# Kernel optimization log

Measured on AMD Instinct MI355X. Metric: run time of the kernel, lower is better.

The kernel has to match this reference:

```python
import jax, jax.numpy as jnp
import numpy as np

N_NODES = 100000
N_EDGES = 1600000
F_IN = 256
HIDDEN = 32
HEADS = 4
N_CLASSES = 16
NEG_SLOPE = 0.2  # PyG GATConv default


def setup_inputs() -> dict:
    key = jax.random.key(0)
    ks = jax.random.split(key, 10)
    x = jax.random.normal(ks[0], (N_NODES, F_IN), dtype=jnp.float32)
    edge_index = jax.random.randint(ks[1], (2, N_EDGES), 0, N_NODES, dtype=jnp.int64)
    # layer 1 params: W1 [F_IN, HEADS*HIDDEN], attention vectors [HEADS, HIDDEN]
    s1 = 1.0 / np.sqrt(F_IN)
    W1 = jax.random.uniform(ks[2], (F_IN, HEADS * HIDDEN), jnp.float32, -s1, s1)
    a_src1 = jax.random.normal(ks[3], (HEADS, HIDDEN), dtype=jnp.float32) * 0.1
    a_dst1 = jax.random.normal(ks[4], (HEADS, HIDDEN), dtype=jnp.float32) * 0.1
    b1 = jnp.zeros((HEADS * HIDDEN,), jnp.float32)
    # layer 2 params: in = HEADS*HIDDEN, out = N_CLASSES, heads=1
    d2 = HEADS * HIDDEN
    s2 = 1.0 / np.sqrt(d2)
    W2 = jax.random.uniform(ks[5], (d2, N_CLASSES), jnp.float32, -s2, s2)
    a_src2 = jax.random.normal(ks[6], (1, N_CLASSES), dtype=jnp.float32) * 0.1
    a_dst2 = jax.random.normal(ks[7], (1, N_CLASSES), dtype=jnp.float32) * 0.1
    b2 = jnp.zeros((N_CLASSES,), jnp.float32)
    return {"x": x, "W1": W1, "a_src1": a_src1, "a_dst1": a_dst1, "b1": b1,
            "W2": W2, "a_src2": a_src2, "a_dst2": a_dst2, "b2": b2,
            "edge_index": edge_index}


def gat_conv(x, src, dst, W, a_src, a_dst, bias, heads, head_dim, concat, num_nodes):
    # linear transform: [N, K, H]
    h = (x @ W).reshape(num_nodes, heads, head_dim)
    # per-node attention logits: [N, K]
    alpha_src = jnp.einsum('nkh,kh->nk', h, a_src)
    alpha_dst = jnp.einsum('nkh,kh->nk', h, a_dst)
    # per-edge scores (message src -> dst): [E, K]
    e = jax.nn.leaky_relu(alpha_src[src] + alpha_dst[dst], NEG_SLOPE)
    # segment softmax grouped by destination node (stable)
    m = jax.ops.segment_max(e, dst, num_segments=num_nodes)
    ex = jnp.exp(e - m[dst])
    denom = jax.ops.segment_sum(ex, dst, num_segments=num_nodes)
    alpha = ex / (denom[dst] + 1e-16)  # [E, K]
    # weighted scatter-add aggregation: [N, K, H]
    msg = h[src] * alpha[:, :, None]
    out = jax.ops.segment_sum(msg, dst, num_segments=num_nodes)
    if concat:
        return out.reshape(num_nodes, heads * head_dim) + bias
    return out.mean(axis=1) + bias


def reference(x, W1, a_src1, a_dst1, b1, W2, a_src2, a_dst2, b2, edge_index):
    n = x.shape[0]
    loops = jnp.arange(n, dtype=edge_index.dtype)
    src = jnp.concatenate([edge_index[0], loops])  # PyG adds self-loops
    dst = jnp.concatenate([edge_index[1], loops])
    # eval mode: feature/attention dropout is identity
    h = gat_conv(x, src, dst, W1, a_src1, a_dst1, b1, HEADS, HIDDEN, True, n)
    h = jax.nn.elu(h)
    out = gat_conv(h, src, dst, W2, a_src2, a_dst2, b2, 1, N_CLASSES, False, n)
    return jax.nn.log_softmax(out, axis=1)
```

## Files before the change

### kernel.cpp

```cpp
#include <hip/hip_runtime.h>
#include <hip/hip_bf16.h>
#include <math.h>

#define N_NODES 100000
#define N_EDGES 1600000
#define EP (N_EDGES + N_NODES)
#define F_IN 256
#define HIDDEN 32
#define HEADS 4
#define D1 (HEADS*HIDDEN)
#define NC 16
#define NEG_SLOPE 0.2f
#define NSTRIP 6250
#define NBUCK 391
#define NCHUNKB 128
#define CHUNK 13312

typedef __attribute__((ext_vector_type(8))) short bf16x8;
typedef __attribute__((ext_vector_type(4))) float f32x4;


__device__ __forceinline__ float lrelu(float x) { return x > 0.f ? x : NEG_SLOPE * x; }

__device__ __forceinline__ unsigned bfpack(float lo, float hi) {
    unsigned a = __float_as_uint(lo), b = __float_as_uint(hi);
    a = (a + 0x7fffu + ((a >> 16) & 1u)) >> 16;
    b = (b + 0x7fffu + ((b >> 16) & 1u)) & 0xffff0000u;
    return a | b;
}
__device__ __forceinline__ unsigned short bf16r(float f) {
    unsigned a = __float_as_uint(f);
    return (unsigned short)((a + 0x7fffu + ((a >> 16) & 1u)) >> 16);
}
__device__ __forceinline__ float bflo(unsigned v) { return __uint_as_float(v << 16); }
__device__ __forceinline__ float bfhi(unsigned v) { return __uint_as_float(v & 0xffff0000u); }

__global__ __launch_bounds__(256) void kA_hist(const int* __restrict__ ei,
                                               unsigned* __restrict__ histG) {
    __shared__ unsigned h[NBUCK];
    const int tid = threadIdx.x;
    for (int i = tid; i < NBUCK; i += 256) h[i] = 0;
    __syncthreads();
    const int base = blockIdx.x * CHUNK;
    const int lim = min(base + CHUNK, EP);
    for (int e = base + tid * 4; e + 3 < lim; e += 1024) {
        if (e < N_EDGES) {
            const int4 d = *(const int4*)(ei + N_EDGES + e);
            atomicAdd(&h[d.x >> 8], 1u);
            atomicAdd(&h[d.y >> 8], 1u);
            atomicAdd(&h[d.z >> 8], 1u);
            atomicAdd(&h[d.w >> 8], 1u);
        } else {
            const int dst = e - N_EDGES;
            atomicAdd(&h[dst >> 8], 1u);
            atomicAdd(&h[(dst + 1) >> 8], 1u);
            atomicAdd(&h[(dst + 2) >> 8], 1u);
            atomicAdd(&h[(dst + 3) >> 8], 1u);
        }
    }
    __syncthreads();
    for (int i = tid; i < NBUCK; i += 256) histG[i * NCHUNKB + blockIdx.x] = h[i];
}

__global__ __launch_bounds__(512) void kB_scan(unsigned* __restrict__ histG,
                                               int* __restrict__ row_ptr) {
    __shared__ unsigned sb[512];
    const int t = threadIdx.x;
    unsigned total = 0;
    if (t < NBUCK) {
        const uint4* p = (const uint4*)(histG + t * NCHUNKB);
        #pragma unroll
        for (int c = 0; c < NCHUNKB / 4; ++c) {
            const uint4 v = p[c];
            total += v.x + v.y + v.z + v.w;
        }
    }
    sb[t] = (t < NBUCK) ? total : 0;
    __syncthreads();
    for (int off = 1; off < 512; off <<= 1) {
        const unsigned u = (t >= off) ? sb[t - off] : 0;
        __syncthreads();
        sb[t] += u;
        __syncthreads();
    }
    if (t < NBUCK) {
        unsigned run = sb[t] - total;
        uint4* p = (uint4*)(histG + t * NCHUNKB);
        #pragma unroll
        for (int c = 0; c < NCHUNKB / 4; ++c) {
            uint4 v = p[c];
            uint4 o;
            o.x = run; run += v.x;
            o.y = run; run += v.y;
            o.z = run; run += v.z;
            o.w = run; run += v.w;
            p[c] = o;
        }
    }
    if (t == 0) row_ptr[N_NODES] = EP;
}

__global__ __launch_bounds__(256) void kC_bucket(const int* __restrict__ ei,
                                                 const unsigned* __restrict__ histG,
                                                 unsigned* __restrict__ packed) {
    __shared__ unsigned cur[NBUCK];
    const int tid = threadIdx.x;
    for (int i = tid; i < NBUCK; i += 256) cur[i] = histG[i * NCHUNKB + blockIdx.x];
    __syncthreads();
    const int base = blockIdx.x * CHUNK;
    const int lim = min(base + CHUNK, EP);
    for (int e = base + tid * 4; e + 3 < lim; e += 1024) {
        int4 s, d;
        if (e < N_EDGES) {
            s = *(const int4*)(ei + e);
            d = *(const int4*)(ei + N_EDGES + e);
        } else {
            s = make_int4(e - N_EDGES, e + 1 - N_EDGES, e + 2 - N_EDGES, e + 3 - N_EDGES);
            d = s;
        }
        unsigned p0 = atomicAdd(&cur[d.x >> 8], 1u);
        packed[p0] = ((unsigned)s.x << 8) | ((unsigned)d.x & 255u);
        unsigned p1 = atomicAdd(&cur[d.y >> 8], 1u);
        packed[p1] = ((unsigned)s.y << 8) | ((unsigned)d.y & 255u);
        unsigned p2 = atomicAdd(&cur[d.z >> 8], 1u);
        packed[p2] = ((unsigned)s.z << 8) | ((unsigned)d.z & 255u);
        unsigned p3 = atomicAdd(&cur[d.w >> 8], 1u);
        packed[p3] = ((unsigned)s.w << 8) | ((unsigned)d.w & 255u);
    }
}

__global__ __launch_bounds__(256) void kD_sort(const unsigned* __restrict__ histG,
                                               const unsigned* __restrict__ packed,
                                               int* __restrict__ row_ptr,
                                               int* __restrict__ csr_src) {
    __shared__ unsigned hist[256];
    __shared__ unsigned sb[256];
    __shared__ unsigned cur[256];
    const int b = blockIdx.x, tid = threadIdx.x;
    const unsigned start = histG[b * NCHUNKB];
    const unsigned end = (b + 1 < NBUCK) ? histG[(b + 1) * NCHUNKB] : (unsigned)EP;
    hist[tid] = 0;
    __syncthreads();
    for (unsigned i = start + tid; i < end; i += 256)
        atomicAdd(&hist[packed[i] & 255u], 1u);
    __syncthreads();
    const unsigned v = hist[tid];
    sb[tid] = v;
    __syncthreads();
    for (int off = 1; off < 256; off <<= 1) {
        const unsigned u = (tid >= off) ? sb[tid - off] : 0;
        __syncthreads();
        sb[tid] += u;
        __syncthreads();
    }
    const unsigned pos0 = start + sb[tid] - v;
    cur[tid] = pos0;
    const int node = b * 256 + tid;
    if (node < N_NODES) row_ptr[node] = (int)pos0;
    __syncthreads();
    for (unsigned i = start + tid; i < end; i += 256) {
        const unsigned pv = packed[i];
        const unsigned pos = atomicAdd(&cur[pv & 255u], 1u);
        csr_src[pos] = (int)(pv >> 8);
    }
}

__global__ __launch_bounds__(128) void k_w1t(const float* __restrict__ W1,
                                             unsigned short* __restrict__ W1T) {
    const int k = blockIdx.x;
    const int n = threadIdx.x;
    W1T[n * 256 + k] = bf16r(W1[k * 128 + n]);
}

__global__ __launch_bounds__(256) void k_gemm1m(
    const float* __restrict__ x, const unsigned short* __restrict__ W1T,
    const float* __restrict__ a_src1, const float* __restrict__ a_dst1,
    unsigned* __restrict__ h1b, float* __restrict__ as1, float* __restrict__ ad1)
{
    const int s = blockIdx.x * 4 + (threadIdx.x >> 6);
    if (s >= NSTRIP) return;
    const int lane = threadIdx.x & 63;
    const int q = lane & 15, g = lane >> 4;
    const int base = s * 16;
    const int row = base + q;
    const int kseg = g * 8;

    f32x4 acc[8];
    #pragma unroll
    for (int t = 0; t < 8; ++t) acc[t] = (f32x4){0.f, 0.f, 0.f, 0.f};

    #pragma unroll
    for (int kk = 0; kk < 8; ++kk) {
        const float4* xp = (const float4*)(x + (size_t)row * 256 + kk * 32 + kseg);
        const float4 xa = xp[0], xb = xp[1];
        union { unsigned u[4]; bf16x8 v; } A;
        A.u[0] = bfpack(xa.x, xa.y);
        A.u[1] = bfpack(xa.z, xa.w);
        A.u[2] = bfpack(xb.x, xb.y);
        A.u[3] = bfpack(xb.z, xb.w);
        #pragma unroll
        for (int t = 0; t < 8; ++t) {
            const bf16x8 B = *(const bf16x8*)(W1T + (size_t)(t * 16 + q) * 256 + kk * 32 + kseg);
            acc[t] = __builtin_amdgcn_mfma_f32_16x16x32_bf16(A.v, B, acc[t], 0, 0, 0);
        }
    }

    float ps[4][4], pd[4][4];
    #pragma unroll
    for (int h = 0; h < 4; ++h)
        #pragma unroll
        for (int r = 0; r < 4; ++r) { ps[h][r] = 0.f; pd[h][r] = 0.f; }
    #pragma unroll
    for (int t = 0; t < 8; ++t) {
        const int col = t * 16 + q;
        const float av = a_src1[col];
        const float dv = a_dst1[col];
        const int h = t >> 1;
        #pragma unroll
        for (int r = 0; r < 4; ++r) {
            ps[h][r] = fmaf(acc[t][r], av, ps[h][r]);
            pd[h][r] = fmaf(acc[t][r], dv, pd[h][r]);
        }
    }
    #pragma unroll
    for (int mask = 1; mask < 16; mask <<= 1) {
        #pragma unroll
        for (int h = 0; h < 4; ++h)
            #pragma unroll
            for (int r = 0; r < 4; ++r) {
                ps[h][r] += __shfl_xor(ps[h][r], mask);
                pd[h][r] += __shfl_xor(pd[h][r], mask);
            }
    }
    #pragma unroll
    for (int h = 0; h < 4; ++h)
        #pragma unroll
        for (int r = 0; r < 4; ++r)
            if (q == h * 4 + r) {
                const int n = base + g * 4 + r;
                as1[n * 4 + h] = ps[h][r];
                ad1[n * 4 + h] = pd[h][r];
            }

    #pragma unroll
    for (int t = 0; t < 8; ++t) {
        #pragma unroll
        for (int r = 0; r < 4; ++r) {
            const float other = __shfl_xor(acc[t][r], 1);
            if (!(q & 1)) {
                const int n = base + g * 4 + r;
                h1b[(size_t)n * 64 + t * 8 + (q >> 1)] = bfpack(acc[t][r], other);
            }
        }
    }
}

__global__ __launch_bounds__(256) void k_agg1f(
    const int* __restrict__ row_ptr, const int* __restrict__ csr_src,
    const float* __restrict__ as1, const float* __restrict__ ad1,
    const unsigned* __restrict__ h1b, float* __restrict__ agg1)
{
    const int dst  = blockIdx.x * 4 + (threadIdx.x >> 6);
    const int lane = threadIdx.x & 63;
    const int start = row_ptr[dst], end = row_ptr[dst + 1];

    const int eh = lane >> 2;
    const int k  = lane & 3;
    const float adk = ad1[dst * 4 + k];
    float m = -1e30f, den = 0.f;
    for (int i = start + eh; i < end; i += 16) {
        const int src = csr_src[i];
        const float s = lrelu(as1[src * 4 + k] + adk);
        const float M = fmaxf(m, s);
        den = den * __expf(m - M) + __expf(s - M);
        m = M;
    }
    #pragma unroll
    for (int mask = 4; mask < 64; mask <<= 1) {
        const float mo = __shfl_xor(m, mask);
        const float dn = __shfl_xor(den, mask);
        const float M  = fmaxf(m, mo);
        den = den * __expf(m - M) + dn * __expf(mo - M);
        m = M;
    }

    const int hw = lane >> 5;
    const int c  = lane & 31;
    const int oh = c >> 3;
    const float mh   = __shfl(m, oh);
    const float rden = 1.f / (__shfl(den, oh) + 1e-16f);
    const float adh  = ad1[dst * 4 + oh];

    float4 acc = make_float4(0.f, 0.f, 0.f, 0.f);
    const uint2* h1v = (const uint2*)h1b;
    int i = start + hw;
    for (; i + 2 < end; i += 4) {
        const int s0 = csr_src[i], s1 = csr_src[i + 2];
        const float e0 = lrelu(as1[s0 * 4 + oh] + adh);
        const float e1 = lrelu(as1[s1 * 4 + oh] + adh);
        const uint2 v0 = h1v[(size_t)s0 * 32 + c];
        const uint2 v1 = h1v[(size_t)s1 * 32 + c];
        const float a0 = __expf(e0 - mh) * rden;
        const float a1 = __expf(e1 - mh) * rden;
        acc.x = fmaf(a0, bflo(v0.x), acc.x); acc.y = fmaf(a0, bfhi(v0.x), acc.y);
        acc.z = fmaf(a0, bflo(v0.y), acc.z); acc.w = fmaf(a0, bfhi(v0.y), acc.w);
        acc.x = fmaf(a1, bflo(v1.x), acc.x); acc.y = fmaf(a1, bfhi(v1.x), acc.y);
        acc.z = fmaf(a1, bflo(v1.y), acc.z); acc.w = fmaf(a1, bfhi(v1.y), acc.w);
    }
    if (i < end) {
        const int s0 = csr_src[i];
        const float e0 = lrelu(as1[s0 * 4 + oh] + adh);
        const uint2 v0 = h1v[(size_t)s0 * 32 + c];
        const float a0 = __expf(e0 - mh) * rden;
        acc.x = fmaf(a0, bflo(v0.x), acc.x); acc.y = fmaf(a0, bfhi(v0.x), acc.y);
        acc.z = fmaf(a0, bflo(v0.y), acc.z); acc.w = fmaf(a0, bfhi(v0.y), acc.w);
    }
    acc.x += __shfl_xor(acc.x, 32);
    acc.y += __shfl_xor(acc.y, 32);
    acc.z += __shfl_xor(acc.z, 32);
    acc.w += __shfl_xor(acc.w, 32);
    if (hw == 0) ((float4*)agg1)[(size_t)dst * 32 + c] = acc;
}

__global__ __launch_bounds__(256) void k_gemm2(
    const float* __restrict__ agg1, const float* __restrict__ b1,
    const float* __restrict__ W2, const float* __restrict__ a_src2,
    const float* __restrict__ a_dst2,
    float* __restrict__ h2, float* __restrict__ as2, float* __restrict__ ad2)
{
    __shared__ float w2s[128 * 16];
    __shared__ float xs2[16 * 132];
    const int tid = threadIdx.x;
    const int base = blockIdx.x * 16;
    {
        const float4* wb = (const float4*)W2;
        float4* wd = (float4*)w2s;
        #pragma unroll
        for (int i = 0; i < 2; ++i) wd[tid + i * 256] = wb[tid + i * 256];
    }
    #pragma unroll
    for (int i = 0; i < 2; ++i) {
        const int idx = tid + i * 256;
        const int nl = idx >> 5;
        const int c4 = idx & 31;
        float4 v = ((const float4*)(agg1 + (size_t)(base + nl) * 128))[c4];
        const float4 b = ((const float4*)b1)[c4];
        v.x += b.x; v.y += b.y; v.z += b.z; v.w += b.w;
        v.x = v.x > 0.f ? v.x : expm1f(v.x);
        v.y = v.y > 0.f ? v.y : expm1f(v.y);
        v.z = v.z > 0.f ? v.z : expm1f(v.z);
        v.w = v.w > 0.f ? v.w : expm1f(v.w);
        *((float4*)(xs2 + nl * 132 + c4 * 4)) = v;
    }
    __syncthreads();
    const int nl = tid >> 4, c = tid & 15;
    float acc = 0.f;
    #pragma unroll
    for (int k = 0; k < 128; ++k)
        acc = fmaf(xs2[nl * 132 + k], w2s[k * 16 + c], acc);
    const int n = base + nl;
    h2[(size_t)n * 16 + c] = acc;
    float ps = acc * a_src2[c];
    float pd = acc * a_dst2[c];
    ps += __shfl_xor(ps, 1); ps += __shfl_xor(ps, 2); ps += __shfl_xor(ps, 4); ps += __shfl_xor(ps, 8);
    pd += __shfl_xor(pd, 1); pd += __shfl_xor(pd, 2); pd += __shfl_xor(pd, 4); pd += __shfl_xor(pd, 8);
    if (c == 0) { as2[n] = ps; ad2[n] = pd; }
}

__global__ __launch_bounds__(256) void k_agg2f(
    const int* __restrict__ row_ptr, const int* __restrict__ csr_src,
    const float* __restrict__ as2, const float* __restrict__ ad2,
    const float* __restrict__ h2, float* __restrict__ agg2)
{
    const int dst  = blockIdx.x * 16 + (threadIdx.x >> 4);
    const int lane = threadIdx.x & 15;
    const int start = row_ptr[dst], end = row_ptr[dst + 1];
    const float add = ad2[dst];

    float m = -1e30f, den = 0.f;
    for (int i = start + lane; i < end; i += 16) {
        const float s = lrelu(as2[csr_src[i]] + add);
        const float M = fmaxf(m, s);
        den = den * __expf(m - M) + __expf(s - M);
        m = M;
    }
    #pragma unroll
    for (int mask = 1; mask < 16; mask <<= 1) {
        const float mo = __shfl_xor(m, mask);
        const float dn = __shfl_xor(den, mask);
        const float M  = fmaxf(m, mo);
        den = den * __expf(m - M) + dn * __expf(mo - M);
        m = M;
    }
    const float rden = 1.f / (den + 1e-16f);

    float acc = 0.f;
    for (int i = start; i < end; ++i) {
        const int src = csr_src[i];
        const float s = lrelu(as2[src] + add);
        const float a = __expf(s - m) * rden;
        acc = fmaf(a, h2[(size_t)src * 16 + lane], acc);
    }
    agg2[(size_t)dst * 16 + lane] = acc;
}

__global__ __launch_bounds__(256) void k_out(
    const float* __restrict__ agg2, const float* __restrict__ b2,
    float* __restrict__ out)
{
    const int tid = threadIdx.x;
    const int n = blockIdx.x * 16 + (tid >> 4);
    const int c = tid & 15;
    const float v = agg2[(size_t)n * 16 + c] + b2[c];
    float m = v;
    m = fmaxf(m, __shfl_xor(m, 1)); m = fmaxf(m, __shfl_xor(m, 2));
    m = fmaxf(m, __shfl_xor(m, 4)); m = fmaxf(m, __shfl_xor(m, 8));
    float s = expf(v - m);
    s += __shfl_xor(s, 1); s += __shfl_xor(s, 2);
    s += __shfl_xor(s, 4); s += __shfl_xor(s, 8);
    out[(size_t)n * 16 + c] = v - m - logf(s);
}

extern "C" void kernel_launch(void* const* d_in, const int* in_sizes, int n_in,
                              void* d_out, int out_size, void* d_ws, size_t ws_size,
                              hipStream_t stream) {
    const float* x      = (const float*)d_in[0];
    const float* W1     = (const float*)d_in[1];
    const float* a_src1 = (const float*)d_in[2];
    const float* a_dst1 = (const float*)d_in[3];
    const float* b1     = (const float*)d_in[4];
    const float* W2     = (const float*)d_in[5];
    const float* a_src2 = (const float*)d_in[6];
    const float* a_dst2 = (const float*)d_in[7];
    const float* b2     = (const float*)d_in[8];
    const int*   ei     = (const int*)d_in[9];
    float* out = (float*)d_out;
    char* ws = (char*)d_ws;

    unsigned* h1b   = (unsigned*)(ws + 0);
    float* agg1     = (float*)(ws + 51200000);
    float* as1      = (float*)(ws + 102400000);
    float* ad1      = (float*)(ws + 104000000);
    int*   row_ptr  = (int*)(ws + 105600000);
    unsigned* histG = (unsigned*)(ws + 106000016);
    int*   csr_src  = (int*)(ws + 106402064);
    unsigned short* W1T = (unsigned short*)(ws + 113202064);
    unsigned* packed = (unsigned*)(ws + 113267600);
    float* h2   = (float*)(ws + 0);
    float* as2  = (float*)(ws + 6400000);
    float* ad2  = (float*)(ws + 6800000);
    float* agg2 = (float*)(ws + 7200000);

    k_w1t<<<256, 128, 0, stream>>>(W1, W1T);
    k_gemm1m<<<1563, 256, 0, stream>>>(x, W1T, a_src1, a_dst1, h1b, as1, ad1);

    kA_hist<<<NCHUNKB, 256, 0, stream>>>(ei, histG);
    kB_scan<<<1, 512, 0, stream>>>(histG, row_ptr);
    kC_bucket<<<NCHUNKB, 256, 0, stream>>>(ei, histG, packed);
    kD_sort<<<NBUCK, 256, 0, stream>>>(histG, packed, row_ptr, csr_src);

    k_agg1f<<<25000, 256, 0, stream>>>(row_ptr, csr_src, as1, ad1, h1b, agg1);

    k_gemm2<<<6250, 256, 0, stream>>>(agg1, b1, W2, a_src2, a_dst2, h2, as2, ad2);
    k_agg2f<<<6250, 256, 0, stream>>>(row_ptr, csr_src, as2, ad2, h2, agg2);
    k_out<<<6250, 256, 0, stream>>>(agg2, b2, out);
}
```

Before: 488.5 us.

## Stage GEMM1 x tiles via LDS, store agg1 and h2 as bf16, widen gathers

The first GEMM now stages each block's 64 input rows into swizzled shared memory with direct global-to-LDS loads before the MFMA loop, instead of per-lane global loads. The layer-1 aggregation uses 16-byte gathers with four edge groups per wave and writes its output as packed bf16, which halves the agg1 traffic read by the second GEMM. The layer-2 features h2 are also stored as bf16, and the layer-2 aggregation is unrolled by two. Together these cut memory traffic, at the cost of more bf16 rounding in intermediates and 64KB of LDS per GEMM block, which limits occupancy.

```diff
diff --git a/kernel.cpp b/kernel.cpp
--- a/kernel.cpp
+++ b/kernel.cpp
@@ -34,6 +34,13 @@
 }
 __device__ __forceinline__ float bflo(unsigned v) { return __uint_as_float(v << 16); }
 __device__ __forceinline__ float bfhi(unsigned v) { return __uint_as_float(v & 0xffff0000u); }
+
+__device__ __forceinline__ void gload_lds16(const void* g, void* l) {
+    __builtin_amdgcn_global_load_lds(
+        (const __attribute__((address_space(1))) unsigned*)g,
+        (__attribute__((address_space(3))) unsigned*)l,
+        16, 0, 0);
+}
 
 __global__ __launch_bounds__(256) void kA_hist(const int* __restrict__ ei,
                                                unsigned* __restrict__ histG) {
@@ -177,79 +184,97 @@
     const float* __restrict__ a_src1, const float* __restrict__ a_dst1,
     unsigned* __restrict__ h1b, float* __restrict__ as1, float* __restrict__ ad1)
 {
-    const int s = blockIdx.x * 4 + (threadIdx.x >> 6);
-    if (s >= NSTRIP) return;
+    __shared__ float xs[64 * 256];
+    const int wv = threadIdx.x >> 6;
     const int lane = threadIdx.x & 63;
-    const int q = lane & 15, g = lane >> 4;
+    const int s = blockIdx.x * 4 + wv;
     const int base = s * 16;
-    const int row = base + q;
-    const int kseg = g * 8;
-
-    f32x4 acc[8];
+
     #pragma unroll
-    for (int t = 0; t < 8; ++t) acc[t] = (f32x4){0.f, 0.f, 0.f, 0.f};
-
-    #pragma unroll
-    for (int kk = 0; kk < 8; ++kk) {
-        const float4* xp = (const float4*)(x + (size_t)row * 256 + kk * 32 + kseg);
-        const float4 xa = xp[0], xb = xp[1];
-        union { unsigned u[4]; bf16x8 v; } A;
-        A.u[0] = bfpack(xa.x, xa.y);
-        A.u[1] = bfpack(xa.z, xa.w);
-        A.u[2] = bfpack(xb.x, xb.y);
-        A.u[3] = bfpack(xb.z, xb.w);
-        #pragma unroll
-        for (int t = 0; t < 8; ++t) {
-            const bf16x8 B = *(const bf16x8*)(W1T + (size_t)(t * 16 + q) * 256 + kk * 32 + kseg);
-            acc[t] = __builtin_amdgcn_mfma_f32_16x16x32_bf16(A.v, B, acc[t], 0, 0, 0);
-        }
-    }
-
-    float ps[4][4], pd[4][4];
-    #pragma unroll
-    for (int h = 0; h < 4; ++h)
-        #pragma unroll
-        for (int r = 0; r < 4; ++r) { ps[h][r] = 0.f; pd[h][r] = 0.f; }
-    #pragma unroll
-    for (int t = 0; t < 8; ++t) {
-        const int col = t * 16 + q;
-        const float av = a_src1[col];
-        const float dv = a_dst1[col];
-        const int h = t >> 1;
-        #pragma unroll
-        for (int r = 0; r < 4; ++r) {
-            ps[h][r] = fmaf(acc[t][r], av, ps[h][r]);
-            pd[h][r] = fmaf(acc[t][r], dv, pd[h][r]);
-        }
-    }
-    #pragma unroll
-    for (int mask = 1; mask < 16; mask <<= 1) {
+    for (int i = 0; i < 16; ++i) {
+        const int r = wv * 16 + i;
+        int grow = blockIdx.x * 64 + r;
+        if (grow >= N_NODES) grow = N_NODES - 1;
+        const unsigned gr = (unsigned)lane ^ (unsigned)(r & 7);
+        const char* gsrc = (const char*)(x + (size_t)grow * 256) + gr * 16;
+        gload_lds16(gsrc, (char*)xs + r * 1024);
+    }
+    __syncthreads();
+
+    if (s < NSTRIP) {
+        const int q = lane & 15, g = lane >> 4;
+        const int kseg = g * 8;
+        const int rowb = (wv * 16 + q) * 1024;
+        const int sw = q & 7;
+
+        f32x4 acc[8];
+        #pragma unroll
+        for (int t = 0; t < 8; ++t) acc[t] = (f32x4){0.f, 0.f, 0.f, 0.f};
+
+        #pragma unroll
+        for (int kk = 0; kk < 8; ++kk) {
+            const int u = kk * 8 + g * 2;
+            const int ua = (u ^ sw) * 16;
+            const float4 f0 = *(const float4*)((const char*)xs + rowb + ua);
+            const float4 f1 = *(const float4*)((const char*)xs + rowb + (ua ^ 16));
+            union { unsigned u4[4]; bf16x8 v; } A;
+            A.u4[0] = bfpack(f0.x, f0.y);
+            A.u4[1] = bfpack(f0.z, f0.w);
+            A.u4[2] = bfpack(f1.x, f1.y);
+            A.u4[3] = bfpack(f1.z, f1.w);
+            #pragma unroll
+            for (int t = 0; t < 8; ++t) {
+                const bf16x8 B = *(const bf16x8*)(W1T + (size_t)(t * 16 + q) * 256 + kk * 32 + kseg);
+                acc[t] = __builtin_amdgcn_mfma_f32_16x16x32_bf16(A.v, B, acc[t], 0, 0, 0);
+            }
+        }
+
+        float ps[4][4], pd[4][4];
         #pragma unroll
         for (int h = 0; h < 4; ++h)
             #pragma unroll
+            for (int r = 0; r < 4; ++r) { ps[h][r] = 0.f; pd[h][r] = 0.f; }
+        #pragma unroll
+        for (int t = 0; t < 8; ++t) {
+            const int col = t * 16 + q;
+            const float av = a_src1[col];
+            const float dv = a_dst1[col];
+            const int h = t >> 1;
+            #pragma unroll
             for (int r = 0; r < 4; ++r) {
-                ps[h][r] += __shfl_xor(ps[h][r], mask);
-                pd[h][r] += __shfl_xor(pd[h][r], mask);
+                ps[h][r] = fmaf(acc[t][r], av, ps[h][r]);
+                pd[h][r] = fmaf(acc[t][r], dv, pd[h][r]);
             }
-    }
-    #pragma unroll
-    for (int h = 0; h < 4; ++h)
-        #pragma unroll
-        for (int r = 0; r < 4; ++r)
-            if (q == h * 4 + r) {
-                const int n = base + g * 4 + r;
-                as1[n * 4 + h] = ps[h][r];
-                ad1[n * 4 + h] = pd[h][r];
-            }
-
-    #pragma unroll
-    for (int t = 0; t < 8; ++t) {
-        #pragma unroll
-        for (int r = 0; r < 4; ++r) {
-            const float other = __shfl_xor(acc[t][r], 1);
-            if (!(q & 1)) {
-                const int n = base + g * 4 + r;
-                h1b[(size_t)n * 64 + t * 8 + (q >> 1)] = bfpack(acc[t][r], other);
+        }
+        #pragma unroll
+        for (int mask = 1; mask < 16; mask <<= 1) {
+            #pragma unroll
+            for (int h = 0; h < 4; ++h)
+                #pragma unroll
+                for (int r = 0; r < 4; ++r) {
+                    ps[h][r] += __shfl_xor(ps[h][r], mask);
+                    pd[h][r] += __shfl_xor(pd[h][r], mask);
+                }
+        }
+        #pragma unroll
+        for (int h = 0; h < 4; ++h)
+            #pragma unroll
+            for (int r = 0; r < 4; ++r)
+                if (q == h * 4 + r) {
+                    const int n = base + g * 4 + r;
+                    as1[n * 4 + h] = ps[h][r];
+                    ad1[n * 4 + h] = pd[h][r];
+                }
+
+        #pragma unroll
+        for (int t = 0; t < 8; ++t) {
+            #pragma unroll
+            for (int r = 0; r < 4; ++r) {
+                const float other = __shfl_xor(acc[t][r], 1);
+                if (!(q & 1)) {
+                    const int n = base + g * 4 + r;
+                    h1b[(size_t)n * 64 + t * 8 + (q >> 1)] = bfpack(acc[t][r], other);
+                }
             }
         }
     }
@@ -258,7 +283,7 @@
 __global__ __launch_bounds__(256) void k_agg1f(
     const int* __restrict__ row_ptr, const int* __restrict__ csr_src,
     const float* __restrict__ as1, const float* __restrict__ ad1,
-    const unsigned* __restrict__ h1b, float* __restrict__ agg1)
+    const unsigned* __restrict__ h1b, unsigned* __restrict__ agg1b)
 {
     const int dst  = blockIdx.x * 4 + (threadIdx.x >> 6);
     const int lane = threadIdx.x & 63;
@@ -270,9 +295,9 @@
     float m = -1e30f, den = 0.f;
     for (int i = start + eh; i < end; i += 16) {
         const int src = csr_src[i];
-        const float s = lrelu(as1[src * 4 + k] + adk);
-        const float M = fmaxf(m, s);
-        den = den * __expf(m - M) + __expf(s - M);
+        const float sv = lrelu(as1[src * 4 + k] + adk);
+        const float M = fmaxf(m, sv);
+        den = den * __expf(m - M) + __expf(sv - M);
         m = M;
     }
     #pragma unroll
@@ -284,49 +309,65 @@
         m = M;
     }
 
-    const int hw = lane >> 5;
-    const int c  = lane & 31;
-    const int oh = c >> 3;
+    const int ql = lane >> 4;
+    const int c  = lane & 15;
+    const int oh = c >> 2;
     const float mh   = __shfl(m, oh);
     const float rden = 1.f / (__shfl(den, oh) + 1e-16f);
     const float adh  = ad1[dst * 4 + oh];
 
-    float4 acc = make_float4(0.f, 0.f, 0.f, 0.f);
-    const uint2* h1v = (const uint2*)h1b;
-    int i = start + hw;
-    for (; i + 2 < end; i += 4) {
-        const int s0 = csr_src[i], s1 = csr_src[i + 2];
+    float acc[8];
+    #pragma unroll
+    for (int j = 0; j < 8; ++j) acc[j] = 0.f;
+    const uint4* h1v = (const uint4*)h1b;
+    int i = start + ql;
+    for (; i + 4 < end; i += 8) {
+        const int s0 = csr_src[i], s1 = csr_src[i + 4];
         const float e0 = lrelu(as1[s0 * 4 + oh] + adh);
         const float e1 = lrelu(as1[s1 * 4 + oh] + adh);
-        const uint2 v0 = h1v[(size_t)s0 * 32 + c];
-        const uint2 v1 = h1v[(size_t)s1 * 32 + c];
-        const float a0 = __expf(e0 - mh) * rden;
-        const float a1 = __expf(e1 - mh) * rden;
-        acc.x = fmaf(a0, bflo(v0.x), acc.x); acc.y = fmaf(a0, bfhi(v0.x), acc.y);
-        acc.z = fmaf(a0, bflo(v0.y), acc.z); acc.w = fmaf(a0, bfhi(v0.y), acc.w);
-        acc.x = fmaf(a1, bflo(v1.x), acc.x); acc.y = fmaf(a1, bfhi(v1.x), acc.y);
-        acc.z = fmaf(a1, bflo(v1.y), acc.z); acc.w = fmaf(a1, bfhi(v1.y), acc.w);
+        const uint4 v0 = h1v[(size_t)s0 * 16 + c];
+        const uint4 v1 = h1v[(size_t)s1 * 16 + c];
+        const float w0 = __expf(e0 - mh) * rden;
+        const float w1 = __expf(e1 - mh) * rden;
+        acc[0] = fmaf(w0, bflo(v0.x), acc[0]); acc[1] = fmaf(w0, bfhi(v0.x), acc[1]);
+        acc[2] = fmaf(w0, bflo(v0.y), acc[2]); acc[3] = fmaf(w0, bfhi(v0.y), acc[3]);
+        acc[4] = fmaf(w0, bflo(v0.z), acc[4]); acc[5] = fmaf(w0, bfhi(v0.z), acc[5]);
+        acc[6] = fmaf(w0, bflo(v0.w), acc[6]); acc[7] = fmaf(w0, bfhi(v0.w), acc[7]);
+        acc[0] = fmaf(w1, bflo(v1.x), acc[0]); acc[1] = fmaf(w1, bfhi(v1.x), acc[1]);
+        acc[2] = fmaf(w1, bflo(v1.y), acc[2]); acc[3] = fmaf(w1, bfhi(v1.y), acc[3]);
+        acc[4] = fmaf(w1, bflo(v1.z), acc[4]); acc[5] = fmaf(w1, bfhi(v1.z), acc[5]);
+        acc[6] = fmaf(w1, bflo(v1.w), acc[6]); acc[7] = fmaf(w1, bfhi(v1.w), acc[7]);
     }
     if (i < end) {
         const int s0 = csr_src[i];
         const float e0 = lrelu(as1[s0 * 4 + oh] + adh);
-        const uint2 v0 = h1v[(size_t)s0 * 32 + c];
-        const float a0 = __expf(e0 - mh) * rden;
-        acc.x = fmaf(a0, bflo(v0.x), acc.x); acc.y = fmaf(a0, bfhi(v0.x), acc.y);
-        acc.z = fmaf(a0, bflo(v0.y), acc.z); acc.w = fmaf(a0, bfhi(v0.y), acc.w);
-    }
-    acc.x += __shfl_xor(acc.x, 32);
-    acc.y += __shfl_xor(acc.y, 32);
-    acc.z += __shfl_xor(acc.z, 32);
-    acc.w += __shfl_xor(acc.w, 32);
-    if (hw == 0) ((float4*)agg1)[(size_t)dst * 32 + c] = acc;
+        const uint4 v0 = h1v[(size_t)s0 * 16 + c];
+        const float w0 = __expf(e0 - mh) * rden;
+        acc[0] = fmaf(w0, bflo(v0.x), acc[0]); acc[1] = fmaf(w0, bfhi(v0.x), acc[1]);
+        acc[2] = fmaf(w0, bflo(v0.y), acc[2]); acc[3] = fmaf(w0, bfhi(v0.y), acc[3]);
+        acc[4] = fmaf(w0, bflo(v0.z), acc[4]); acc[5] = fmaf(w0, bfhi(v0.z), acc[5]);
+        acc[6] = fmaf(w0, bflo(v0.w), acc[6]); acc[7] = fmaf(w0, bfhi(v0.w), acc[7]);
+    }
+    #pragma unroll
+    for (int j = 0; j < 8; ++j) {
+        acc[j] += __shfl_xor(acc[j], 16);
+        acc[j] += __shfl_xor(acc[j], 32);
+    }
+    if (ql == 0) {
+        uint4 o;
+        o.x = bfpack(acc[0], acc[1]);
+        o.y = bfpack(acc[2], acc[3]);
+        o.z = bfpack(acc[4], acc[5]);
+        o.w = bfpack(acc[6], acc[7]);
+        ((uint4*)agg1b)[(size_t)dst * 16 + c] = o;
+    }
 }
 
 __global__ __launch_bounds__(256) void k_gemm2(
-    const float* __restrict__ agg1, const float* __restrict__ b1,
+    const unsigned* __restrict__ agg1b, const float* __restrict__ b1,
     const float* __restrict__ W2, const float* __restrict__ a_src2,
     const float* __restrict__ a_dst2,
-    float* __restrict__ h2, float* __restrict__ as2, float* __restrict__ ad2)
+    unsigned* __restrict__ h2b, float* __restrict__ as2, float* __restrict__ ad2)
 {
     __shared__ float w2s[128 * 16];
     __shared__ float xs2[16 * 132];
@@ -338,19 +379,20 @@
         #pragma unroll
         for (int i = 0; i < 2; ++i) wd[tid + i * 256] = wb[tid + i * 256];
     }
-    #pragma unroll
-    for (int i = 0; i < 2; ++i) {
-        const int idx = tid + i * 256;
-        const int nl = idx >> 5;
-        const int c4 = idx & 31;
-        float4 v = ((const float4*)(agg1 + (size_t)(base + nl) * 128))[c4];
-        const float4 b = ((const float4*)b1)[c4];
-        v.x += b.x; v.y += b.y; v.z += b.z; v.w += b.w;
-        v.x = v.x > 0.f ? v.x : expm1f(v.x);
-        v.y = v.y > 0.f ? v.y : expm1f(v.y);
-        v.z = v.z > 0.f ? v.z : expm1f(v.z);
-        v.w = v.w > 0.f ? v.w : expm1f(v.w);
-        *((float4*)(xs2 + nl * 132 + c4 * 4)) = v;
+    {
+        const int row = tid >> 4;
+        const int u = tid & 15;
+        const uint4 v = ((const uint4*)agg1b)[(size_t)(base + row) * 16 + u];
+        const float4 bb0 = ((const float4*)b1)[u * 2];
+        const float4 bb1 = ((const float4*)b1)[u * 2 + 1];
+        float e[8] = { bflo(v.x) + bb0.x, bfhi(v.x) + bb0.y,
+                       bflo(v.y) + bb0.z, bfhi(v.y) + bb0.w,
+                       bflo(v.z) + bb1.x, bfhi(v.z) + bb1.y,
+                       bflo(v.w) + bb1.z, bfhi(v.w) + bb1.w };
+        #pragma unroll
+        for (int j = 0; j < 8; ++j) e[j] = e[j] > 0.f ? e[j] : expm1f(e[j]);
+        #pragma unroll
+        for (int j = 0; j < 8; ++j) xs2[row * 132 + u * 8 + j] = e[j];
     }
     __syncthreads();
     const int nl = tid >> 4, c = tid & 15;
@@ -359,7 +401,8 @@
     for (int k = 0; k < 128; ++k)
         acc = fmaf(xs2[nl * 132 + k], w2s[k * 16 + c], acc);
     const int n = base + nl;
-    h2[(size_t)n * 16 + c] = acc;
+    const float other = __shfl_xor(acc, 1);
+    if (!(c & 1)) h2b[(size_t)n * 8 + (c >> 1)] = bfpack(acc, other);
     float ps = acc * a_src2[c];
     float pd = acc * a_dst2[c];
     ps += __shfl_xor(ps, 1); ps += __shfl_xor(ps, 2); ps += __shfl_xor(ps, 4); ps += __shfl_xor(ps, 8);
@@ -370,7 +413,7 @@
 __global__ __launch_bounds__(256) void k_agg2f(
     const int* __restrict__ row_ptr, const int* __restrict__ csr_src,
     const float* __restrict__ as2, const float* __restrict__ ad2,
-    const float* __restrict__ h2, float* __restrict__ agg2)
+    const unsigned* __restrict__ h2b, float* __restrict__ agg2)
 {
     const int dst  = blockIdx.x * 16 + (threadIdx.x >> 4);
     const int lane = threadIdx.x & 15;
@@ -379,9 +422,9 @@
 
     float m = -1e30f, den = 0.f;
     for (int i = start + lane; i < end; i += 16) {
-        const float s = lrelu(as2[csr_src[i]] + add);
-        const float M = fmaxf(m, s);
-        den = den * __expf(m - M) + __expf(s - M);
+        const float sv = lrelu(as2[csr_src[i]] + add);
+        const float M = fmaxf(m, sv);
+        den = den * __expf(m - M) + __expf(sv - M);
         m = M;
     }
     #pragma unroll
@@ -395,11 +438,25 @@
     const float rden = 1.f / (den + 1e-16f);
 
     float acc = 0.f;
-    for (int i = start; i < end; ++i) {
-        const int src = csr_src[i];
-        const float s = lrelu(as2[src] + add);
-        const float a = __expf(s - m) * rden;
-        acc = fmaf(a, h2[(size_t)src * 16 + lane], acc);
+    const unsigned hsel = lane >> 1;
+    int i = start;
+    for (; i + 1 < end; i += 2) {
+        const int s0 = csr_src[i], s1 = csr_src[i + 1];
+        const float e0 = lrelu(as2[s0] + add);
+        const float e1 = lrelu(as2[s1] + add);
+        const unsigned hv0 = h2b[(size_t)s0 * 8 + hsel];
+        const unsigned hv1 = h2b[(size_t)s1 * 8 + hsel];
+        const float w0 = __expf(e0 - m) * rden;
+        const float w1 = __expf(e1 - m) * rden;
+        acc = fmaf(w0, (lane & 1) ? bfhi(hv0) : bflo(hv0), acc);
+        acc = fmaf(w1, (lane & 1) ? bfhi(hv1) : bflo(hv1), acc);
+    }
+    if (i < end) {
+        const int s0 = csr_src[i];
+        const float e0 = lrelu(as2[s0] + add);
+        const unsigned hv0 = h2b[(size_t)s0 * 8 + hsel];
+        const float w0 = __expf(e0 - m) * rden;
+        acc = fmaf(w0, (lane & 1) ? bfhi(hv0) : bflo(hv0), acc);
     }
     agg2[(size_t)dst * 16 + lane] = acc;
 }
@@ -438,7 +495,7 @@
     char* ws = (char*)d_ws;
 
     unsigned* h1b   = (unsigned*)(ws + 0);
-    float* agg1     = (float*)(ws + 51200000);
+    unsigned* agg1b = (unsigned*)(ws + 51200000);
     float* as1      = (float*)(ws + 102400000);
     float* ad1      = (float*)(ws + 104000000);
     int*   row_ptr  = (int*)(ws + 105600000);
@@ -446,7 +503,7 @@
     int*   csr_src  = (int*)(ws + 106402064);
     unsigned short* W1T = (unsigned short*)(ws + 113202064);
     unsigned* packed = (unsigned*)(ws + 113267600);
-    float* h2   = (float*)(ws + 0);
+    unsigned* h2b  = (unsigned*)(ws + 0);
     float* as2  = (float*)(ws + 6400000);
     float* ad2  = (float*)(ws + 6800000);
     float* agg2 = (float*)(ws + 7200000);
@@ -459,9 +516,9 @@
     kC_bucket<<<NCHUNKB, 256, 0, stream>>>(ei, histG, packed);
     kD_sort<<<NBUCK, 256, 0, stream>>>(histG, packed, row_ptr, csr_src);
 
-    k_agg1f<<<25000, 256, 0, stream>>>(row_ptr, csr_src, as1, ad1, h1b, agg1);
-
-    k_gemm2<<<6250, 256, 0, stream>>>(agg1, b1, W2, a_src2, a_dst2, h2, as2, ad2);
-    k_agg2f<<<6250, 256, 0, stream>>>(row_ptr, csr_src, as2, ad2, h2, agg2);
+    k_agg1f<<<25000, 256, 0, stream>>>(row_ptr, csr_src, as1, ad1, h1b, agg1b);
+
+    k_gemm2<<<6250, 256, 0, stream>>>(agg1b, b1, W2, a_src2, a_dst2, h2b, as2, ad2);
+    k_agg2f<<<6250, 256, 0, stream>>>(row_ptr, csr_src, as2, ad2, h2b, agg2);
     k_out<<<6250, 256, 0, stream>>>(agg2, b2, out);
 }
```

Result: faster. 452.8 us (-7.3%).
